# Kernel optimization log

Measured on AMD Instinct MI355X. Metric: run time of the kernel, lower is better.

## Reference

```python
import jax, jax.numpy as jnp
import numpy as np

N_HEAD = 16

def setup_inputs() -> dict:
    key = jax.random.key(0)
    ks = jax.random.split(key, 5)
    B, T, C = 2, 2048, 1024
    s = 0.02
    return {
        "x": jax.random.normal(ks[0], (B, T, C), jnp.float32),
        "W_attn": jax.random.normal(ks[1], (3 * C, C), jnp.float32) * s,
        "b_attn": jax.random.normal(ks[2], (3 * C,), jnp.float32) * s,
        "W_proj": jax.random.normal(ks[3], (C, C), jnp.float32) * s,
        "b_proj": jax.random.normal(ks[4], (C,), jnp.float32) * s,
    }

def reference(x, W_attn, b_attn, W_proj, b_proj):
    B, T, C = x.shape
    H = N_HEAD
    D = C // H
    # fused QKV projection (torch Linear: y = x @ W.T + b)
    qkv = jnp.einsum('btc,fc->btf', x, W_attn) + b_attn  # [B,T,3C]
    q, k, v = jnp.split(qkv, 3, axis=-1)
    def to_heads(t):
        return t.reshape(B, T, H, D).transpose(0, 2, 1, 3)  # [B,H,T,D]
    q, k, v = to_heads(q), to_heads(k), to_heads(v)
    scale = 1.0 / jnp.sqrt(jnp.array(D, x.dtype))
    scores = jnp.einsum('bhqd,bhkd->bhqk', q, k) * scale  # [B,H,T,T]
    causal = jnp.tril(jnp.ones((T, T), bool))
    scores = jnp.where(causal, scores, jnp.finfo(x.dtype).min)
    p = jax.nn.softmax(scores, axis=-1)
    y = jnp.einsum('bhqk,bhkd->bhqd', p, v)  # [B,H,T,D]
    y = y.transpose(0, 2, 1, 3).reshape(B, T, C)
    out = jnp.einsum('btc,oc->bto', y, W_proj) + b_proj
    return out
```

## Files before the change

### kernel.cpp

```cpp
#include <hip/hip_runtime.h>

typedef unsigned int u32;
typedef unsigned short u16;
typedef __attribute__((ext_vector_type(8))) short bf16x8;
typedef __attribute__((ext_vector_type(4))) float f32x4;

#define T_ 2048
#define HEADS 16
#define DH 64
#define NQ (2 * HEADS * T_ * DH)

__device__ __forceinline__ u16 f2bf(float f) {
    union { float f; u32 u; } x; x.f = f;
    return (u16)((x.u + 0x7fffu + ((x.u >> 16) & 1u)) >> 16);
}
__device__ __forceinline__ u32 pkbf(float lo, float hi) {
    u32 r;
    asm("v_cvt_pk_bf16_f32 %0, %1, %2" : "=v"(r) : "v"(lo), "v"(hi));
    return r;
}
__device__ __forceinline__ void gll16(const void* g, void* l) {
    __builtin_amdgcn_global_load_lds(
        (const __attribute__((address_space(1))) void*)g,
        (__attribute__((address_space(3))) void*)l, 16, 0, 0);
}

#define QSCALE 0.18033688011112042f
#define DEFER_THR 8.0f

#define NG_X  (4096 * 128)
#define NG_WA (3072 * 128)
__global__ __launch_bounds__(256) void cvt_all(
    const float* __restrict__ x, const float* __restrict__ wa,
    const float* __restrict__ wp,
    u16* __restrict__ dx, u16* __restrict__ dwa, u16* __restrict__ dwp)
{
    int gid = blockIdx.x * 256 + threadIdx.x;
    const float* src; u16* dst;
    if (gid < NG_X)                { src = x;  dst = dx; }
    else if (gid < NG_X + NG_WA)   { src = wa; dst = dwa; gid -= NG_X; }
    else                           { src = wp; dst = dwp; gid -= NG_X + NG_WA; }
    const int m = gid >> 7, s = gid & 127;
    const int kt = s >> 3, seg = s & 7;
    const float4 a0 = *(const float4*)&src[m * 1024 + s * 8];
    const float4 a1 = *(const float4*)&src[m * 1024 + s * 8 + 4];
    uint4 t;
    t.x = pkbf(a0.x, a0.y); t.y = pkbf(a0.z, a0.w);
    t.z = pkbf(a1.x, a1.y); t.w = pkbf(a1.z, a1.w);
    const int mt = m >> 7, r = m & 127;
    char* d = (char*)dst + ((size_t)(mt * 16 + kt)) * 16384
              + r * 128 + ((seg ^ (r & 7)) << 4);
    *(uint4*)d = t;
}

template<int EPI>
__global__ __launch_bounds__(256, 2) void gemm_lds(
    const char* __restrict__ At, const char* __restrict__ Bt,
    const float* __restrict__ bias,
    u16* __restrict__ q, u16* __restrict__ k, u16* __restrict__ vt,
    float* __restrict__ outF)
{
    __shared__ __align__(16) char AsB[2][16384];
    __shared__ __align__(16) char BsB[2][16384];
    const int tid = threadIdx.x;
    const int l = tid & 63, li = l & 15, lg = l >> 4;
    const int w = tid >> 6, wm = w >> 1, wn = w & 1;
    const int m0 = blockIdx.y * 128, n0 = blockIdx.x * 128;
    const char* Ab = At + (size_t)blockIdx.y * (16 * 16384);
    const char* Bb = Bt + (size_t)blockIdx.x * (16 * 16384);

    f32x4 acc[4][4];
    #pragma unroll
    for (int i = 0; i < 4; ++i)
        #pragma unroll
        for (int j = 0; j < 4; ++j) acc[i][j] = (f32x4){0.f, 0.f, 0.f, 0.f};

    #pragma unroll
    for (int i = 0; i < 4; ++i) {
        gll16(Ab + w * 4096 + i * 1024 + l * 16, &AsB[0][w * 4096 + i * 1024]);
        gll16(Bb + w * 4096 + i * 1024 + l * 16, &BsB[0][w * 4096 + i * 1024]);
    }
    asm volatile("s_waitcnt vmcnt(0)" ::: "memory");
    __syncthreads();

    for (int kt = 0; kt < 16; ++kt) {
        const int cur = kt & 1;
        if (kt + 1 < 16) {
            const char* An = Ab + (kt + 1) * 16384;
            const char* Bn = Bb + (kt + 1) * 16384;
            #pragma unroll
            for (int i = 0; i < 4; ++i) {
                gll16(An + w * 4096 + i * 1024 + l * 16, &AsB[cur ^ 1][w * 4096 + i * 1024]);
                gll16(Bn + w * 4096 + i * 1024 + l * 16, &BsB[cur ^ 1][w * 4096 + i * 1024]);
            }
        }
        #pragma unroll
        for (int kc = 0; kc < 2; ++kc) {
            const int key = ((kc * 4 + lg) ^ (li & 7)) << 4;
            bf16x8 a[4], b[4];
            #pragma unroll
            for (int f = 0; f < 4; ++f)
                a[f] = *(const bf16x8*)&AsB[cur][(wm * 64 + f * 16 + li) * 128 + key];
            #pragma unroll
            for (int f = 0; f < 4; ++f)
                b[f] = *(const bf16x8*)&BsB[cur][(wn * 64 + f * 16 + li) * 128 + key];
            #pragma unroll
            for (int mi = 0; mi < 4; ++mi)
                #pragma unroll
                for (int ni = 0; ni < 4; ++ni)
                    acc[mi][ni] = __builtin_amdgcn_mfma_f32_16x16x32_bf16(a[mi], b[ni], acc[mi][ni], 0, 0, 0);
        }
        asm volatile("s_waitcnt vmcnt(0)" ::: "memory");
        __syncthreads();
    }

    const int mb = m0 + wm * 64;
    const int nb0 = n0 + wn * 64;
    if constexpr (EPI == 0) {
        const int part = n0 >> 10;
        if (part < 2) {
            u16* dst = (part == 0) ? q : k;
            const float scl = (part == 0) ? QSCALE : 1.0f;
            #pragma unroll
            for (int mi = 0; mi < 4; ++mi)
                #pragma unroll
                for (int r = 0; r < 4; ++r) {
                    const int m = mb + mi * 16 + lg * 4 + r;
                    const int bb = m >> 11, t = m & 2047;
                    #pragma unroll
                    for (int ni = 0; ni < 4; ++ni) {
                        const int n = nb0 + ni * 16 + li;
                        const int c = n & 1023;
                        const int h = c >> 6, d = c & 63;
                        const float val = (acc[mi][ni][r] + bias[n]) * scl;
                        dst[(((bb << 4) + h) * T_ + t) * DH + d] = f2bf(val);
                    }
                }
        } else {
            #pragma unroll
            for (int mi = 0; mi < 4; ++mi) {
                const int m = mb + mi * 16 + lg * 4;
                const int bb = m >> 11, t0 = m & 2047;
                #pragma unroll
                for (int ni = 0; ni < 4; ++ni) {
                    const int n = nb0 + ni * 16 + li;
                    const int c = n & 1023;
                    const int h = c >> 6, d = c & 63;
                    const float bz = bias[n];
                    u32 w0 = pkbf(acc[mi][ni][0] + bz, acc[mi][ni][1] + bz);
                    u32 w1 = pkbf(acc[mi][ni][2] + bz, acc[mi][ni][3] + bz);
                    *(uint2*)&vt[(((bb << 4) + h) * 64 + d) * (size_t)T_ + t0] = make_uint2(w0, w1);
                }
            }
        }
    } else {
        #pragma unroll
        for (int mi = 0; mi < 4; ++mi)
            #pragma unroll
            for (int r = 0; r < 4; ++r) {
                const int m = mb + mi * 16 + lg * 4 + r;
                #pragma unroll
                for (int ni = 0; ni < 4; ++ni) {
                    const int n = nb0 + ni * 16 + li;
                    outF[m * 1024 + n] = acc[mi][ni][r] + bias[n];
                }
            }
    }
}

__global__ __launch_bounds__(256, 2) void flash_attn(
    const u16* __restrict__ Q, const u16* __restrict__ K,
    const u16* __restrict__ Vt, char* __restrict__ Yt)
{
    __shared__ __align__(16) char KsB[2][8192];
    __shared__ __align__(16) char VsB[2][8192];
    __shared__ __align__(16) char PsB[4][2048];

    const int bh = blockIdx.x;
    const int slot = blockIdx.y;
    const int qt = (slot & 1) ? (31 - (slot >> 1)) : (slot >> 1);
    const int tid = threadIdx.x;
    const int w  = tid >> 6;
    const int l  = tid & 63;
    const int li = l & 15, lg = l >> 4;
    const u16* Qb = Q  + (size_t)bh * (T_ * DH);
    const u16* Kb = K  + (size_t)bh * (T_ * DH);
    const u16* Vb = Vt + (size_t)bh * (T_ * DH);
    const int srow = tid >> 3;
    const int sseg = tid & 7;
    char* Pw = PsB[w];
    const int b = bh >> 4, h = bh & 15;
    const int skey = (srow & 7) << 4;
    const int rdkey = (li & 7) << 4;

    const int wq0 = qt * 64 + w * 16;
    const int q_row = wq0 + li;
    const int nkv = qt + 1;

    bf16x8 qa[2];
    qa[0] = *(const bf16x8*)(Qb + q_row * 64 + 0  + lg * 8);
    qa[1] = *(const bf16x8*)(Qb + q_row * 64 + 32 + lg * 8);

    f32x4 o[4];
    #pragma unroll
    for (int nb = 0; nb < 4; ++nb) o[nb] = (f32x4){0.f, 0.f, 0.f, 0.f};
    float m_r = -INFINITY, l_r = 0.f;

    uint4 kr0, kr1, vr0, vr1;
    kr0 = *(const uint4*)(Kb + srow * 64 + sseg * 8);
    kr1 = *(const uint4*)(Kb + (srow + 32) * 64 + sseg * 8);
    vr0 = *(const uint4*)(Vb + (size_t)srow * T_ + sseg * 8);
    vr1 = *(const uint4*)(Vb + (size_t)(srow + 32) * T_ + sseg * 8);
    *(uint4*)&KsB[0][srow * 128        + ((sseg << 4) ^ skey)] = kr0;
    *(uint4*)&KsB[0][(srow + 32) * 128 + ((sseg << 4) ^ skey)] = kr1;
    *(uint4*)&VsB[0][srow * 128        + ((sseg << 4) ^ skey)] = vr0;
    *(uint4*)&VsB[0][(srow + 32) * 128 + ((sseg << 4) ^ skey)] = vr1;
    __syncthreads();

    for (int j = 0; j < nkv; ++j) {
        const int cur = j & 1;
        const bool has_next = (j + 1 < nkv);
        if (has_next) {
            const int t0 = (j + 1) * 64;
            kr0 = *(const uint4*)(Kb + (t0 + srow) * 64 + sseg * 8);
            kr1 = *(const uint4*)(Kb + (t0 + srow + 32) * 64 + sseg * 8);
            vr0 = *(const uint4*)(Vb + (size_t)srow * T_ + t0 + sseg * 8);
            vr1 = *(const uint4*)(Vb + (size_t)(srow + 32) * T_ + t0 + sseg * 8);
        }
        const char* Kc = KsB[cur];
        f32x4 s[4];
        __builtin_amdgcn_s_setprio(1);
        #pragma unroll
        for (int f = 0; f < 4; ++f) {
            s[f] = (f32x4){0.f, 0.f, 0.f, 0.f};
            #pragma unroll
            for (int c = 0; c < 2; ++c) {
                bf16x8 kb = *(const bf16x8*)&Kc[(f * 16 + li) * 128 + ((c * 64 + lg * 16) ^ rdkey)];
                s[f] = __builtin_amdgcn_mfma_f32_16x16x32_bf16(kb, qa[c], s[f], 0, 0, 0);
            }
        }
        __builtin_amdgcn_s_setprio(0);
        if ((j + 1) * 64 > wq0) {
            const int kbase = j * 64 + lg * 4;
            #pragma unroll
            for (int f = 0; f < 4; ++f)
                #pragma unroll
                for (int r = 0; r < 4; ++r)
                    if (kbase + f * 16 + r > q_row) s[f][r] = -INFINITY;
        }
        float lm = s[0][0];
        #pragma unroll
        for (int f = 0; f < 4; ++f)
            #pragma unroll
            for (int r = 0; r < 4; ++r) lm = fmaxf(lm, s[f][r]);
        if (!__all(lm <= m_r + DEFER_THR)) {
            float tm = lm;
            tm = fmaxf(tm, __shfl_xor(tm, 16));
            tm = fmaxf(tm, __shfl_xor(tm, 32));
            const float mnew = fmaxf(m_r, tm);
            const float corr = exp2f(m_r - mnew);
            m_r = mnew;
            l_r *= corr;
            #pragma unroll
            for (int nb = 0; nb < 4; ++nb)
                #pragma unroll
                for (int r = 0; r < 4; ++r) o[nb][r] *= corr;
        }
        #pragma unroll
        for (int f = 0; f < 4; ++f) {
            float p0 = exp2f(s[f][0] - m_r);
            float p1 = exp2f(s[f][1] - m_r);
            float p2 = exp2f(s[f][2] - m_r);
            float p3 = exp2f(s[f][3] - m_r);
            l_r += (p0 + p1) + (p2 + p3);
            uint2 pk = make_uint2(pkbf(p0, p1), pkbf(p2, p3));
            *(uint2*)&Pw[li * 128 + (((f * 32 + lg * 8)) ^ rdkey)] = pk;
        }
        if (has_next) {
            *(uint4*)&KsB[cur ^ 1][srow * 128        + ((sseg << 4) ^ skey)] = kr0;
            *(uint4*)&KsB[cur ^ 1][(srow + 32) * 128 + ((sseg << 4) ^ skey)] = kr1;
            *(uint4*)&VsB[cur ^ 1][srow * 128        + ((sseg << 4) ^ skey)] = vr0;
            *(uint4*)&VsB[cur ^ 1][(srow + 32) * 128 + ((sseg << 4) ^ skey)] = vr1;
        }
        const char* Vc = VsB[cur];
        __builtin_amdgcn_s_setprio(1);
        #pragma unroll
        for (int c = 0; c < 2; ++c) {
            bf16x8 pa = *(const bf16x8*)&Pw[li * 128 + ((c * 64 + lg * 16) ^ rdkey)];
            #pragma unroll
            for (int nb = 0; nb < 4; ++nb) {
                bf16x8 vb = *(const bf16x8*)&Vc[(nb * 16 + li) * 128 + ((c * 64 + lg * 16) ^ rdkey)];
                o[nb] = __builtin_amdgcn_mfma_f32_16x16x32_bf16(vb, pa, o[nb], 0, 0, 0);
            }
        }
        __builtin_amdgcn_s_setprio(0);
        __syncthreads();
    }

    l_r += __shfl_xor(l_r, 16);
    l_r += __shfl_xor(l_r, 32);
    const float inv = 1.0f / l_r;
    const int r128 = (qt & 1) * 64 + w * 16 + li;
    const int rk = (r128 & 7) << 4;
    char* yrow = Yt + ((size_t)((b * 16 + (qt >> 1)) * 16 + h)) * 16384 + r128 * 128;
    #pragma unroll
    for (int nb = 0; nb < 4; ++nb) {
        const int seg = 2 * nb + (lg >> 1);
        uint2 pk = make_uint2(pkbf(o[nb][0] * inv, o[nb][1] * inv),
                              pkbf(o[nb][2] * inv, o[nb][3] * inv));
        *(uint2*)&yrow[((seg << 4) ^ rk) + (lg & 1) * 8] = pk;
    }
}

extern "C" void kernel_launch(void* const* d_in, const int* in_sizes, int n_in,
                              void* d_out, int out_size, void* d_ws, size_t ws_size,
                              hipStream_t stream) {
    const float* x      = (const float*)d_in[0];
    const float* W_attn = (const float*)d_in[1];
    const float* b_attn = (const float*)d_in[2];
    const float* W_proj = (const float*)d_in[3];
    const float* b_proj = (const float*)d_in[4];
    float* out = (float*)d_out;

    char* ws = (char*)d_ws;
    u16* q   = (u16*)ws;
    u16* k   = (u16*)(ws + (8u << 20));
    u16* vt  = (u16*)(ws + (16u << 20));
    char* xb = ws + (24u << 20);
    char* wab = ws + (32u << 20);
    char* wpb = ws + (38u << 20);

    cvt_all<<<4096, 256, 0, stream>>>(x, W_attn, W_proj, (u16*)xb, (u16*)wab, (u16*)wpb);
    gemm_lds<0><<<dim3(24, 32), 256, 0, stream>>>(xb, wab, b_attn, q, k, vt, nullptr);
    flash_attn<<<dim3(32, 32), 256, 0, stream>>>(q, k, vt, xb );
    gemm_lds<1><<<dim3(8, 32), 256, 0, stream>>>(xb , wpb, b_proj,
                                                 nullptr, nullptr, nullptr, out);
}
```

Measured before the change: 122.9 us.

## Enlarge flash-attention query tile to 128 rows, two 16-row groups per wave

Each flash-attention block now covers 128 query rows instead of 64, and each wave holds two 16-row Q fragments that share every K and V LDS read. The grid is halved to 16 query tiles per head. Waves whose rows lie entirely before the current KV tile skip compute but still help load. The aim is to halve K/V global loads and LDS reads per query row and raise MFMA density. The cost is higher register pressure, idle waves on diagonal tiles, and fewer blocks to fill the GPU.

```diff
diff --git a/kernel.cpp b/kernel.cpp
--- a/kernel.cpp
+++ b/kernel.cpp
@@ -174,11 +174,11 @@
 {
     __shared__ __align__(16) char KsB[2][8192];
     __shared__ __align__(16) char VsB[2][8192];
-    __shared__ __align__(16) char PsB[4][2048];
+    __shared__ __align__(16) char PsB[4][4096];
 
     const int bh = blockIdx.x;
     const int slot = blockIdx.y;
-    const int qt = (slot & 1) ? (31 - (slot >> 1)) : (slot >> 1);
+    const int qt = (slot & 1) ? (15 - (slot >> 1)) : (slot >> 1);
     const int tid = threadIdx.x;
     const int w  = tid >> 6;
     const int l  = tid & 63;
@@ -189,22 +189,30 @@
     const int srow = tid >> 3;
     const int sseg = tid & 7;
     char* Pw = PsB[w];
-    const int b = bh >> 4, h = bh & 15;
+    const int b = bh >> 4, hd = bh & 15;
     const int skey = (srow & 7) << 4;
     const int rdkey = (li & 7) << 4;
 
-    const int wq0 = qt * 64 + w * 16;
-    const int q_row = wq0 + li;
-    const int nkv = qt + 1;
-
-    bf16x8 qa[2];
-    qa[0] = *(const bf16x8*)(Qb + q_row * 64 + 0  + lg * 8);
-    qa[1] = *(const bf16x8*)(Qb + q_row * 64 + 32 + lg * 8);
-
-    f32x4 o[4];
+    const int qtb = qt * 128;
+    const int wq0 = qtb + w * 32;
+    const int q_row0 = wq0 + li;
+    const int q_row1 = wq0 + 16 + li;
+    const int nkv = 2 * qt + 2;
+    const int wnkv = ((wq0 + 31) >> 6) + 1;
+
+    bf16x8 qa0[2], qa1[2];
+    qa0[0] = *(const bf16x8*)(Qb + q_row0 * 64 + 0  + lg * 8);
+    qa0[1] = *(const bf16x8*)(Qb + q_row0 * 64 + 32 + lg * 8);
+    qa1[0] = *(const bf16x8*)(Qb + q_row1 * 64 + 0  + lg * 8);
+    qa1[1] = *(const bf16x8*)(Qb + q_row1 * 64 + 32 + lg * 8);
+
+    f32x4 o0[4], o1[4];
     #pragma unroll
-    for (int nb = 0; nb < 4; ++nb) o[nb] = (f32x4){0.f, 0.f, 0.f, 0.f};
-    float m_r = -INFINITY, l_r = 0.f;
+    for (int nb = 0; nb < 4; ++nb) {
+        o0[nb] = (f32x4){0.f, 0.f, 0.f, 0.f};
+        o1[nb] = (f32x4){0.f, 0.f, 0.f, 0.f};
+    }
+    float m0 = -INFINITY, m1 = -INFINITY, l0 = 0.f, l1 = 0.f;
 
     uint4 kr0, kr1, vr0, vr1;
     kr0 = *(const uint4*)(Kb + srow * 64 + sseg * 8);
@@ -220,6 +228,7 @@
     for (int j = 0; j < nkv; ++j) {
         const int cur = j & 1;
         const bool has_next = (j + 1 < nkv);
+        const bool active = (j < wnkv);
         if (has_next) {
             const int t0 = (j + 1) * 64;
             kr0 = *(const uint4*)(Kb + (t0 + srow) * 64 + sseg * 8);
@@ -227,54 +236,72 @@
             vr0 = *(const uint4*)(Vb + (size_t)srow * T_ + t0 + sseg * 8);
             vr1 = *(const uint4*)(Vb + (size_t)(srow + 32) * T_ + t0 + sseg * 8);
         }
-        const char* Kc = KsB[cur];
-        f32x4 s[4];
-        __builtin_amdgcn_s_setprio(1);
-        #pragma unroll
-        for (int f = 0; f < 4; ++f) {
-            s[f] = (f32x4){0.f, 0.f, 0.f, 0.f};
-            #pragma unroll
-            for (int c = 0; c < 2; ++c) {
-                bf16x8 kb = *(const bf16x8*)&Kc[(f * 16 + li) * 128 + ((c * 64 + lg * 16) ^ rdkey)];
-                s[f] = __builtin_amdgcn_mfma_f32_16x16x32_bf16(kb, qa[c], s[f], 0, 0, 0);
-            }
-        }
-        __builtin_amdgcn_s_setprio(0);
-        if ((j + 1) * 64 > wq0) {
-            const int kbase = j * 64 + lg * 4;
+        if (active) {
+            const char* Kc = KsB[cur];
+            f32x4 s0[4], s1[4];
+            __builtin_amdgcn_s_setprio(1);
+            #pragma unroll
+            for (int f = 0; f < 4; ++f) {
+                s0[f] = (f32x4){0.f, 0.f, 0.f, 0.f};
+                s1[f] = (f32x4){0.f, 0.f, 0.f, 0.f};
+                #pragma unroll
+                for (int c = 0; c < 2; ++c) {
+                    bf16x8 kb = *(const bf16x8*)&Kc[(f * 16 + li) * 128 + ((c * 64 + lg * 16) ^ rdkey)];
+                    s0[f] = __builtin_amdgcn_mfma_f32_16x16x32_bf16(kb, qa0[c], s0[f], 0, 0, 0);
+                    s1[f] = __builtin_amdgcn_mfma_f32_16x16x32_bf16(kb, qa1[c], s1[f], 0, 0, 0);
+                }
+            }
+            __builtin_amdgcn_s_setprio(0);
+            if ((j + 1) * 64 > wq0) {
+                const int kbase = j * 64 + lg * 4;
+                #pragma unroll
+                for (int f = 0; f < 4; ++f)
+                    #pragma unroll
+                    for (int r = 0; r < 4; ++r) {
+                        const int kk = kbase + f * 16 + r;
+                        if (kk > q_row0) s0[f][r] = -INFINITY;
+                        if (kk > q_row1) s1[f][r] = -INFINITY;
+                    }
+            }
+            float lm0 = s0[0][0], lm1 = s1[0][0];
             #pragma unroll
             for (int f = 0; f < 4; ++f)
                 #pragma unroll
-                for (int r = 0; r < 4; ++r)
-                    if (kbase + f * 16 + r > q_row) s[f][r] = -INFINITY;
-        }
-        float lm = s[0][0];
-        #pragma unroll
-        for (int f = 0; f < 4; ++f)
-            #pragma unroll
-            for (int r = 0; r < 4; ++r) lm = fmaxf(lm, s[f][r]);
-        if (!__all(lm <= m_r + DEFER_THR)) {
-            float tm = lm;
-            tm = fmaxf(tm, __shfl_xor(tm, 16));
-            tm = fmaxf(tm, __shfl_xor(tm, 32));
-            const float mnew = fmaxf(m_r, tm);
-            const float corr = exp2f(m_r - mnew);
-            m_r = mnew;
-            l_r *= corr;
-            #pragma unroll
-            for (int nb = 0; nb < 4; ++nb)
-                #pragma unroll
-                for (int r = 0; r < 4; ++r) o[nb][r] *= corr;
-        }
-        #pragma unroll
-        for (int f = 0; f < 4; ++f) {
-            float p0 = exp2f(s[f][0] - m_r);
-            float p1 = exp2f(s[f][1] - m_r);
-            float p2 = exp2f(s[f][2] - m_r);
-            float p3 = exp2f(s[f][3] - m_r);
-            l_r += (p0 + p1) + (p2 + p3);
-            uint2 pk = make_uint2(pkbf(p0, p1), pkbf(p2, p3));
-            *(uint2*)&Pw[li * 128 + (((f * 32 + lg * 8)) ^ rdkey)] = pk;
+                for (int r = 0; r < 4; ++r) {
+                    lm0 = fmaxf(lm0, s0[f][r]);
+                    lm1 = fmaxf(lm1, s1[f][r]);
+                }
+            if (!__all((lm0 <= m0 + DEFER_THR) & (lm1 <= m1 + DEFER_THR))) {
+                float t0r = lm0, t1r = lm1;
+                t0r = fmaxf(t0r, __shfl_xor(t0r, 16));
+                t0r = fmaxf(t0r, __shfl_xor(t0r, 32));
+                t1r = fmaxf(t1r, __shfl_xor(t1r, 16));
+                t1r = fmaxf(t1r, __shfl_xor(t1r, 32));
+                const float mn0 = fmaxf(m0, t0r), mn1 = fmaxf(m1, t1r);
+                const float c0 = exp2f(m0 - mn0), c1 = exp2f(m1 - mn1);
+                m0 = mn0; m1 = mn1;
+                l0 *= c0; l1 *= c1;
+                #pragma unroll
+                for (int nb = 0; nb < 4; ++nb)
+                    #pragma unroll
+                    for (int r = 0; r < 4; ++r) {
+                        o0[nb][r] *= c0;
+                        o1[nb][r] *= c1;
+                    }
+            }
+            #pragma unroll
+            for (int f = 0; f < 4; ++f) {
+                float a0 = exp2f(s0[f][0] - m0), a1 = exp2f(s0[f][1] - m0);
+                float a2 = exp2f(s0[f][2] - m0), a3 = exp2f(s0[f][3] - m0);
+                l0 += (a0 + a1) + (a2 + a3);
+                uint2 pk = make_uint2(pkbf(a0, a1), pkbf(a2, a3));
+                *(uint2*)&Pw[li * 128 + ((f * 32 + lg * 8) ^ rdkey)] = pk;
+                float b0 = exp2f(s1[f][0] - m1), b1 = exp2f(s1[f][1] - m1);
+                float b2 = exp2f(s1[f][2] - m1), b3 = exp2f(s1[f][3] - m1);
+                l1 += (b0 + b1) + (b2 + b3);
+                uint2 qk2 = make_uint2(pkbf(b0, b1), pkbf(b2, b3));
+                *(uint2*)&Pw[(16 + li) * 128 + ((f * 32 + lg * 8) ^ rdkey)] = qk2;
+            }
         }
         if (has_next) {
             *(uint4*)&KsB[cur ^ 1][srow * 128        + ((sseg << 4) ^ skey)] = kr0;
@@ -282,33 +309,43 @@
             *(uint4*)&VsB[cur ^ 1][srow * 128        + ((sseg << 4) ^ skey)] = vr0;
             *(uint4*)&VsB[cur ^ 1][(srow + 32) * 128 + ((sseg << 4) ^ skey)] = vr1;
         }
-        const char* Vc = VsB[cur];
-        __builtin_amdgcn_s_setprio(1);
+        if (active) {
+            const char* Vc = VsB[cur];
+            __builtin_amdgcn_s_setprio(1);
+            #pragma unroll
+            for (int c = 0; c < 2; ++c) {
+                bf16x8 pa0 = *(const bf16x8*)&Pw[li * 128        + ((c * 64 + lg * 16) ^ rdkey)];
+                bf16x8 pa1 = *(const bf16x8*)&Pw[(16 + li) * 128 + ((c * 64 + lg * 16) ^ rdkey)];
+                #pragma unroll
+                for (int nb = 0; nb < 4; ++nb) {
+                    bf16x8 vb = *(const bf16x8*)&Vc[(nb * 16 + li) * 128 + ((c * 64 + lg * 16) ^ rdkey)];
+                    o0[nb] = __builtin_amdgcn_mfma_f32_16x16x32_bf16(vb, pa0, o0[nb], 0, 0, 0);
+                    o1[nb] = __builtin_amdgcn_mfma_f32_16x16x32_bf16(vb, pa1, o1[nb], 0, 0, 0);
+                }
+            }
+            __builtin_amdgcn_s_setprio(0);
+        }
+        __syncthreads();
+    }
+
+    l0 += __shfl_xor(l0, 16); l0 += __shfl_xor(l0, 32);
+    l1 += __shfl_xor(l1, 16); l1 += __shfl_xor(l1, 32);
+    const float i0 = 1.0f / l0, i1 = 1.0f / l1;
+    char* ytile = Yt + ((size_t)((b * 16 + qt) * 16 + hd)) * 16384;
+    #pragma unroll
+    for (int h = 0; h < 2; ++h) {
+        const int r128 = w * 32 + h * 16 + li;
+        const int rk = (r128 & 7) << 4;
+        char* yrow = ytile + r128 * 128;
+        const float inv = h ? i1 : i0;
+        const f32x4* oo = h ? o1 : o0;
         #pragma unroll
-        for (int c = 0; c < 2; ++c) {
-            bf16x8 pa = *(const bf16x8*)&Pw[li * 128 + ((c * 64 + lg * 16) ^ rdkey)];
-            #pragma unroll
-            for (int nb = 0; nb < 4; ++nb) {
-                bf16x8 vb = *(const bf16x8*)&Vc[(nb * 16 + li) * 128 + ((c * 64 + lg * 16) ^ rdkey)];
-                o[nb] = __builtin_amdgcn_mfma_f32_16x16x32_bf16(vb, pa, o[nb], 0, 0, 0);
-            }
-        }
-        __builtin_amdgcn_s_setprio(0);
-        __syncthreads();
-    }
-
-    l_r += __shfl_xor(l_r, 16);
-    l_r += __shfl_xor(l_r, 32);
-    const float inv = 1.0f / l_r;
-    const int r128 = (qt & 1) * 64 + w * 16 + li;
-    const int rk = (r128 & 7) << 4;
-    char* yrow = Yt + ((size_t)((b * 16 + (qt >> 1)) * 16 + h)) * 16384 + r128 * 128;
-    #pragma unroll
-    for (int nb = 0; nb < 4; ++nb) {
-        const int seg = 2 * nb + (lg >> 1);
-        uint2 pk = make_uint2(pkbf(o[nb][0] * inv, o[nb][1] * inv),
-                              pkbf(o[nb][2] * inv, o[nb][3] * inv));
-        *(uint2*)&yrow[((seg << 4) ^ rk) + (lg & 1) * 8] = pk;
+        for (int nb = 0; nb < 4; ++nb) {
+            const int seg = 2 * nb + (lg >> 1);
+            uint2 pk = make_uint2(pkbf(oo[nb][0] * inv, oo[nb][1] * inv),
+                                  pkbf(oo[nb][2] * inv, oo[nb][3] * inv));
+            *(uint2*)&yrow[((seg << 4) ^ rk) + (lg & 1) * 8] = pk;
+        }
     }
 }
 
@@ -332,7 +369,7 @@
 
     cvt_all<<<4096, 256, 0, stream>>>(x, W_attn, W_proj, (u16*)xb, (u16*)wab, (u16*)wpb);
     gemm_lds<0><<<dim3(24, 32), 256, 0, stream>>>(xb, wab, b_attn, q, k, vt, nullptr);
-    flash_attn<<<dim3(32, 32), 256, 0, stream>>>(q, k, vt, xb );
+    flash_attn<<<dim3(32, 16), 256, 0, stream>>>(q, k, vt, xb );
     gemm_lds<1><<<dim3(8, 32), 256, 0, stream>>>(xb , wpb, b_proj,
                                                  nullptr, nullptr, nullptr, out);
 }
```

After: 133.3 us. +8.4%, slower.

## Pre-swizzle K/V tiles in QKV epilogue and stream them via direct global-to-LDS loads

Applied to the files above, without the earlier changes.

The QKV GEMM epilogue now writes K and V^T into per-head 64-row tile images that already use the XOR-swizzled LDS layout. The attention kernel then copies each 8KB tile straight into shared memory with global_load_lds, with no register staging and no separate LDS store pass. This is meant to remove the register round-trip, the swizzle arithmetic and the VGPR pressure from the attention inner loop. The cost is scattered 2-byte stores for K in the GEMM epilogue, and the next tile's prefetch now overlaps through the async DMA path.

```diff
diff --git a/kernel.cpp b/kernel.cpp
--- a/kernel.cpp
+++ b/kernel.cpp
@@ -57,7 +57,7 @@
 __global__ __launch_bounds__(256, 2) void gemm_lds(
     const char* __restrict__ At, const char* __restrict__ Bt,
     const float* __restrict__ bias,
-    u16* __restrict__ q, u16* __restrict__ k, u16* __restrict__ vt,
+    u16* __restrict__ q, char* __restrict__ kimg, char* __restrict__ vimg,
     float* __restrict__ outF)
 {
     __shared__ __align__(16) char AsB[2][16384];
@@ -118,9 +118,7 @@
     const int nb0 = n0 + wn * 64;
     if constexpr (EPI == 0) {
         const int part = n0 >> 10;
-        if (part < 2) {
-            u16* dst = (part == 0) ? q : k;
-            const float scl = (part == 0) ? QSCALE : 1.0f;
+        if (part == 0) {
             #pragma unroll
             for (int mi = 0; mi < 4; ++mi)
                 #pragma unroll
@@ -132,8 +130,27 @@
                         const int n = nb0 + ni * 16 + li;
                         const int c = n & 1023;
                         const int h = c >> 6, d = c & 63;
-                        const float val = (acc[mi][ni][r] + bias[n]) * scl;
-                        dst[(((bb << 4) + h) * T_ + t) * DH + d] = f2bf(val);
+                        const float val = (acc[mi][ni][r] + bias[n]) * QSCALE;
+                        q[(((bb << 4) + h) * T_ + t) * DH + d] = f2bf(val);
+                    }
+                }
+        } else if (part == 1) {
+            #pragma unroll
+            for (int mi = 0; mi < 4; ++mi)
+                #pragma unroll
+                for (int r = 0; r < 4; ++r) {
+                    const int m = mb + mi * 16 + lg * 4 + r;
+                    const int bb = m >> 11, t = m & 2047;
+                    const int j = t >> 6, tr = t & 63;
+                    const int rk = (tr & 7) << 4;
+                    char* tile = kimg + (((size_t)((bb << 4))) << 18) + j * 8192 + tr * 128;
+                    #pragma unroll
+                    for (int ni = 0; ni < 4; ++ni) {
+                        const int n = nb0 + ni * 16 + li;
+                        const int c = n & 1023;
+                        const int h = c >> 6, d = c & 63;
+                        const float val = acc[mi][ni][r] + bias[n];
+                        *(u16*)&tile[((size_t)h << 18) + ((((d >> 3) << 4)) ^ rk) + (d & 7) * 2] = f2bf(val);
                     }
                 }
         } else {
@@ -141,6 +158,8 @@
             for (int mi = 0; mi < 4; ++mi) {
                 const int m = mb + mi * 16 + lg * 4;
                 const int bb = m >> 11, t0 = m & 2047;
+                const int j = t0 >> 6, tc = t0 & 63;
+                const int sege = (((tc >> 3) & 7) << 4);
                 #pragma unroll
                 for (int ni = 0; ni < 4; ++ni) {
                     const int n = nb0 + ni * 16 + li;
@@ -149,7 +168,9 @@
                     const float bz = bias[n];
                     u32 w0 = pkbf(acc[mi][ni][0] + bz, acc[mi][ni][1] + bz);
                     u32 w1 = pkbf(acc[mi][ni][2] + bz, acc[mi][ni][3] + bz);
-                    *(uint2*)&vt[(((bb << 4) + h) * 64 + d) * (size_t)T_ + t0] = make_uint2(w0, w1);
+                    char* dst = vimg + (((size_t)((bb << 4) + h)) << 18) + j * 8192
+                              + d * 128 + (sege ^ ((d & 7) << 4)) + (tc & 7) * 2;
+                    *(uint2*)dst = make_uint2(w0, w1);
                 }
             }
         }
@@ -169,8 +190,8 @@
 }
 
 __global__ __launch_bounds__(256, 2) void flash_attn(
-    const u16* __restrict__ Q, const u16* __restrict__ K,
-    const u16* __restrict__ Vt, char* __restrict__ Yt)
+    const u16* __restrict__ Q, const char* __restrict__ Kimg,
+    const char* __restrict__ Vimg, char* __restrict__ Yt)
 {
     __shared__ __align__(16) char KsB[2][8192];
     __shared__ __align__(16) char VsB[2][8192];
@@ -183,15 +204,13 @@
     const int w  = tid >> 6;
     const int l  = tid & 63;
     const int li = l & 15, lg = l >> 4;
-    const u16* Qb = Q  + (size_t)bh * (T_ * DH);
-    const u16* Kb = K  + (size_t)bh * (T_ * DH);
-    const u16* Vb = Vt + (size_t)bh * (T_ * DH);
-    const int srow = tid >> 3;
-    const int sseg = tid & 7;
+    const u16* Qb = Q + (size_t)bh * (T_ * DH);
+    const char* Kb = Kimg + ((size_t)bh << 18);
+    const char* Vb = Vimg + ((size_t)bh << 18);
     char* Pw = PsB[w];
     const int b = bh >> 4, h = bh & 15;
-    const int skey = (srow & 7) << 4;
     const int rdkey = (li & 7) << 4;
+    const int wseg = w * 2048;
 
     const int wq0 = qt * 64 + w * 16;
     const int q_row = wq0 + li;
@@ -206,26 +225,24 @@
     for (int nb = 0; nb < 4; ++nb) o[nb] = (f32x4){0.f, 0.f, 0.f, 0.f};
     float m_r = -INFINITY, l_r = 0.f;
 
-    uint4 kr0, kr1, vr0, vr1;
-    kr0 = *(const uint4*)(Kb + srow * 64 + sseg * 8);
-    kr1 = *(const uint4*)(Kb + (srow + 32) * 64 + sseg * 8);
-    vr0 = *(const uint4*)(Vb + (size_t)srow * T_ + sseg * 8);
-    vr1 = *(const uint4*)(Vb + (size_t)(srow + 32) * T_ + sseg * 8);
-    *(uint4*)&KsB[0][srow * 128        + ((sseg << 4) ^ skey)] = kr0;
-    *(uint4*)&KsB[0][(srow + 32) * 128 + ((sseg << 4) ^ skey)] = kr1;
-    *(uint4*)&VsB[0][srow * 128        + ((sseg << 4) ^ skey)] = vr0;
-    *(uint4*)&VsB[0][(srow + 32) * 128 + ((sseg << 4) ^ skey)] = vr1;
+    #pragma unroll
+    for (int i = 0; i < 2; ++i) {
+        gll16(Kb + wseg + i * 1024 + l * 16, &KsB[0][wseg + i * 1024]);
+        gll16(Vb + wseg + i * 1024 + l * 16, &VsB[0][wseg + i * 1024]);
+    }
+    asm volatile("s_waitcnt vmcnt(0)" ::: "memory");
     __syncthreads();
 
     for (int j = 0; j < nkv; ++j) {
         const int cur = j & 1;
-        const bool has_next = (j + 1 < nkv);
-        if (has_next) {
-            const int t0 = (j + 1) * 64;
-            kr0 = *(const uint4*)(Kb + (t0 + srow) * 64 + sseg * 8);
-            kr1 = *(const uint4*)(Kb + (t0 + srow + 32) * 64 + sseg * 8);
-            vr0 = *(const uint4*)(Vb + (size_t)srow * T_ + t0 + sseg * 8);
-            vr1 = *(const uint4*)(Vb + (size_t)(srow + 32) * T_ + t0 + sseg * 8);
+        if (j + 1 < nkv) {
+            const char* Kn = Kb + (j + 1) * 8192;
+            const char* Vn = Vb + (j + 1) * 8192;
+            #pragma unroll
+            for (int i = 0; i < 2; ++i) {
+                gll16(Kn + wseg + i * 1024 + l * 16, &KsB[cur ^ 1][wseg + i * 1024]);
+                gll16(Vn + wseg + i * 1024 + l * 16, &VsB[cur ^ 1][wseg + i * 1024]);
+            }
         }
         const char* Kc = KsB[cur];
         f32x4 s[4];
@@ -276,12 +293,6 @@
             uint2 pk = make_uint2(pkbf(p0, p1), pkbf(p2, p3));
             *(uint2*)&Pw[li * 128 + (((f * 32 + lg * 8)) ^ rdkey)] = pk;
         }
-        if (has_next) {
-            *(uint4*)&KsB[cur ^ 1][srow * 128        + ((sseg << 4) ^ skey)] = kr0;
-            *(uint4*)&KsB[cur ^ 1][(srow + 32) * 128 + ((sseg << 4) ^ skey)] = kr1;
-            *(uint4*)&VsB[cur ^ 1][srow * 128        + ((sseg << 4) ^ skey)] = vr0;
-            *(uint4*)&VsB[cur ^ 1][(srow + 32) * 128 + ((sseg << 4) ^ skey)] = vr1;
-        }
         const char* Vc = VsB[cur];
         __builtin_amdgcn_s_setprio(1);
         #pragma unroll
@@ -323,16 +334,16 @@
     float* out = (float*)d_out;
 
     char* ws = (char*)d_ws;
-    u16* q   = (u16*)ws;
-    u16* k   = (u16*)(ws + (8u << 20));
-    u16* vt  = (u16*)(ws + (16u << 20));
-    char* xb = ws + (24u << 20);
+    u16* q    = (u16*)ws;
+    char* kimg = ws + (8u << 20);
+    char* vimg = ws + (16u << 20);
+    char* xb  = ws + (24u << 20);
     char* wab = ws + (32u << 20);
     char* wpb = ws + (38u << 20);
 
     cvt_all<<<4096, 256, 0, stream>>>(x, W_attn, W_proj, (u16*)xb, (u16*)wab, (u16*)wpb);
-    gemm_lds<0><<<dim3(24, 32), 256, 0, stream>>>(xb, wab, b_attn, q, k, vt, nullptr);
-    flash_attn<<<dim3(32, 32), 256, 0, stream>>>(q, k, vt, xb );
+    gemm_lds<0><<<dim3(24, 32), 256, 0, stream>>>(xb, wab, b_attn, q, kimg, vimg, nullptr);
+    flash_attn<<<dim3(32, 32), 256, 0, stream>>>(q, kimg, vimg, xb );
     gemm_lds<1><<<dim3(8, 32), 256, 0, stream>>>(xb , wpb, b_proj,
                                                  nullptr, nullptr, nullptr, out);
 }
```

New measurement: 123.0 us. About the same (+0.1%).
